# Kernel optimization log

Hardware: AMD Instinct MI355X
Metric: run time of the kernel (lower is better)

## Reference

```python
import jax, jax.numpy as jnp
import numpy as np

N = 100_000      # nodes
E = 1_600_000    # edges (avg degree 16)
F_IN = 128       # input features
H = 64           # hidden
C = 40           # classes


def setup_inputs() -> dict:
    key = jax.random.key(0)
    ks = jax.random.split(key, 12)
    s = 0.05
    return {
        "x": jax.random.normal(ks[0], (N, F_IN), dtype=jnp.float32),
        "edge_index": jax.random.randint(ks[1], (2, E), 0, N, dtype=jnp.int64),
        "edge_weight": jax.random.uniform(ks[2], (E,), dtype=jnp.float32),
        # first_lin: Linear(F_IN, H)
        "W_first": jax.random.normal(ks[3], (F_IN, H), dtype=jnp.float32) * s,
        "b_first": jnp.zeros((H,), jnp.float32),
        # convs[0], convs[1]: GCNConv(H, H)
        "W_c1": jax.random.normal(ks[4], (H, H), dtype=jnp.float32) * s,
        "b_c1": jnp.zeros((H,), jnp.float32),
        "W_c2": jax.random.normal(ks[5], (H, H), dtype=jnp.float32) * s,
        "b_c2": jnp.zeros((H,), jnp.float32),
        # lin2: Linear(H, C)
        "W_out": jax.random.normal(ks[6], (H, C), dtype=jnp.float32) * s,
        "b_out": jnp.zeros((C,), jnp.float32),
    }


def gcn_conv(h, edge_weight, row, col, W, b, n):
    """PyG GCNConv: h' = D^-1/2 (A + I) D^-1/2 (h W) + b, with edge weights."""
    h = h @ W                                        # [n, H]
    # add self-loops with weight 1
    loops = jnp.arange(n, dtype=row.dtype)
    row_sl = jnp.concatenate([row, loops])           # source nodes
    col_sl = jnp.concatenate([col, loops])           # target nodes
    ew_sl = jnp.concatenate([edge_weight, jnp.ones((n,), edge_weight.dtype)])
    # symmetric normalization
    deg = jax.ops.segment_sum(ew_sl, col_sl, num_segments=n)
    dinv = jnp.where(deg > 0, jax.lax.rsqrt(jnp.where(deg > 0, deg, 1.0)), 0.0)
    norm = dinv[row_sl] * ew_sl * dinv[col_sl]       # [E+n]
    # gather -> scale -> scatter-add at targets
    msgs = norm[:, None] * h[row_sl]                 # [E+n, H]
    out = jax.ops.segment_sum(msgs, col_sl, num_segments=n)
    return out + b


def reference(x, edge_index, edge_weight, W_first, b_first, W_c1, b_c1,
              W_c2, b_c2, W_out, b_out):
    row, col = edge_index[0], edge_index[1]
    n = x.shape[0]
    h = jax.nn.relu(x @ W_first + b_first)           # first_lin + relu (dropout eval no-op)
    h = jax.nn.relu(gcn_conv(h, edge_weight, row, col, W_c1, b_c1, n))
    h = jax.nn.relu(gcn_conv(h, edge_weight, row, col, W_c2, b_c2, n))
    logits = h @ W_out + b_out                       # lin2
    return jax.nn.log_softmax(logits, axis=-1)
```

## Files before the change

kernel.cpp:

```cpp
#include <hip/hip_runtime.h>
#include <hip/hip_bf16.h>
#include <cstdint>
#include <cstddef>

#define NN 100000
#define NE 1600000
#define FIN 128
#define HD 64
#define NC 40
#define NTILE (NN / 16)
#define MM_BLOCKS ((NTILE + 3) / 4)

#define BUK 256
#define NBUK ((NN + BUK - 1) / BUK)
#define EPB 1024
#define NBLK ((NE + EPB - 1) / EPB)

#define XSTR 68

typedef unsigned short u16;
typedef unsigned int u32;
typedef __attribute__((ext_vector_type(8))) short short8v;
typedef __attribute__((ext_vector_type(4))) float accf4;

__device__ __forceinline__ float u2lo(u32 u) { return __uint_as_float(u << 16); }
__device__ __forceinline__ float u2hi(u32 u) { return __uint_as_float(u & 0xFFFF0000u); }
__device__ __forceinline__ u16 f2b(float f) {
    u32 u = __float_as_uint(f);
    return (u16)((u + 0x7FFFu + ((u >> 16) & 1u)) >> 16);
}
__device__ __forceinline__ u32 pk2(float lo, float hi) {
    return (u32)f2b(lo) | ((u32)f2b(hi) << 16);
}

__launch_bounds__(256)
__global__ void k_build1(const int* __restrict__ ei, u32* __restrict__ hist,
                         const float* __restrict__ x, const float* __restrict__ W,
                         const float* __restrict__ b, u16* __restrict__ out) {
    if (blockIdx.x < NBLK) {
        __shared__ u32 lh[NBUK];
        int blk = blockIdx.x, tid = threadIdx.x;
        for (int i = tid; i < NBUK; i += 256) lh[i] = 0;
        __syncthreads();
        #pragma unroll
        for (int it = 0; it < EPB / 256; it++) {
            int e = blk * EPB + it * 256 + tid;
            if (e < NE) {
                int col = ei[NE + e];
                atomicAdd(&lh[col >> 8], 1u);
            }
        }
        __syncthreads();
        for (int i = tid; i < NBUK; i += 256) hist[(size_t)i * NBLK + blk] = lh[i];
        return;
    }
    __shared__ u32 xs[64 * XSTR];
    int tid = threadIdx.x;
    int bi  = blockIdx.x - NBLK;
    int nodeB = bi * 64;
    const float4* x4 = (const float4*)x;
    for (int idx = tid; idx < 64 * 16; idx += 256) {
        int row = idx >> 4, seg = idx & 15;
        uint4 d = make_uint4(0u, 0u, 0u, 0u);
        if (nodeB + row < NN) {
            float4 a = x4[(size_t)(nodeB + row) * 32 + seg * 2];
            float4 c = x4[(size_t)(nodeB + row) * 32 + seg * 2 + 1];
            d.x = pk2(a.x, a.y);
            d.y = pk2(a.z, a.w);
            d.z = pk2(c.x, c.y);
            d.w = pk2(c.z, c.w);
        }
        *(uint4*)(xs + row * XSTR + seg * 4) = d;
    }
    __syncthreads();
    int lane = tid & 63;
    int wv   = tid >> 6;
    int tile = bi * 4 + wv;
    if (tile >= NTILE) return;
    int row = lane & 15;
    int kg  = lane >> 4;
    short8v bW[4][4];
    #pragma unroll
    for (int kt = 0; kt < 4; kt++)
        #pragma unroll
        for (int ct = 0; ct < 4; ct++)
            #pragma unroll
            for (int j = 0; j < 8; j++)
                bW[kt][ct][j] = (short)f2b(W[(kt*32 + kg*8 + j) * HD + ct*16 + row]);
    int node0 = tile * 16;
    short8v af[4];
    #pragma unroll
    for (int kt = 0; kt < 4; kt++)
        af[kt] = *(const short8v*)(xs + (wv*16 + row) * XSTR + kt * 16 + kg * 4);
    accf4 acc[4] = {};
    #pragma unroll
    for (int kt = 0; kt < 4; kt++)
        #pragma unroll
        for (int ct = 0; ct < 4; ct++)
            acc[ct] = __builtin_amdgcn_mfma_f32_16x16x32_bf16(af[kt], bW[kt][ct], acc[ct], 0, 0, 0);
    #pragma unroll
    for (int ct = 0; ct < 4; ct++) {
        float bias = b[ct*16 + row];
        #pragma unroll
        for (int r = 0; r < 4; r++) {
            float v = fmaxf(acc[ct][r] + bias, 0.f);
            out[(size_t)(node0 + kg*4 + r) * HD + ct*16 + row] = f2b(v);
        }
    }
}

__global__ void k_bscan(u32* __restrict__ hist, u32* __restrict__ bucketTotal) {
    int b = blockIdx.x;
    int lane = threadIdx.x;
    u32* h = hist + (size_t)b * NBLK;
    u32 carry = 0;
    for (int j0 = 0; j0 < NBLK; j0 += 64) {
        int j = j0 + lane;
        u32 v = (j < NBLK) ? h[j] : 0;
        u32 inc = v;
        #pragma unroll
        for (int d = 1; d < 64; d <<= 1) {
            u32 t = __shfl_up(inc, d);
            if (lane >= d) inc += t;
        }
        if (j < NBLK) h[j] = carry + inc - v;
        carry += __shfl(inc, 63);
    }
    if (lane == 0) bucketTotal[b] = carry;
}

__global__ void k_bstart(const u32* __restrict__ bucketTotal, u32* __restrict__ bucketStart,
                         int* __restrict__ off) {
    int lane = threadIdx.x;
    u32 carry = 0;
    for (int j0 = 0; j0 < NBUK; j0 += 64) {
        int j = j0 + lane;
        u32 v = (j < NBUK) ? bucketTotal[j] : 0;
        u32 inc = v;
        #pragma unroll
        for (int d = 1; d < 64; d <<= 1) {
            u32 t = __shfl_up(inc, d);
            if (lane >= d) inc += t;
        }
        if (j < NBUK) bucketStart[j] = carry + inc - v;
        carry += __shfl(inc, 63);
    }
    if (lane == 0) { bucketStart[NBUK] = carry; off[NN] = (int)carry; }
}

__launch_bounds__(256)
__global__ void k_scatter(const int* __restrict__ ei, const float* __restrict__ ew,
                          const u32* __restrict__ hist, const u32* __restrict__ bucketStart,
                          uint2* __restrict__ rec) {
    __shared__ u32 lh[NBUK];
    __shared__ u32 gb[NBUK];
    int blk = blockIdx.x, tid = threadIdx.x;
    for (int i = tid; i < NBUK; i += 256) {
        lh[i] = 0;
        gb[i] = bucketStart[i] + hist[(size_t)i * NBLK + blk];
    }
    __syncthreads();
    #pragma unroll
    for (int it = 0; it < EPB / 256; it++) {
        int e = blk * EPB + it * 256 + tid;
        if (e < NE) {
            int row = ei[e], col = ei[NE + e];
            float wv = ew[e];
            int bkt = col >> 8;
            u32 cl = (u32)(col & 255);
            u32 r = atomicAdd(&lh[bkt], 1u);
            u32 slot = gb[bkt] + r;
            rec[slot] = make_uint2((u32)row | (cl << 24), __float_as_uint(wv));
        }
    }
}

__launch_bounds__(256)
__global__ void k_bucket(const uint2* __restrict__ rec, const u32* __restrict__ bucketStart,
                         float* __restrict__ dinv, int* __restrict__ off,
                         uint2* __restrict__ csr) {
    __shared__ u32 lpk[BUK];
    __shared__ u32 loff[BUK];
    __shared__ u32 wt[4];
    int b = blockIdx.x, tid = threadIdx.x;
    int base = b * BUK;
    u32 seg0 = bucketStart[b], seg1 = bucketStart[b + 1];
    int nb = (int)(seg1 - seg0);
    lpk[tid] = 0;
    __syncthreads();
    for (int idx = tid; idx < nb; idx += 256) {
        uint2 ab = rec[seg0 + idx];
        u32 cl = ab.x >> 24;
        u32 fx = __float2uint_rn(__uint_as_float(ab.y) * 16384.0f);
        atomicAdd(&lpk[cl], (1u << 20) | fx);
    }
    __syncthreads();
    u32 pk = lpk[tid];
    u32 cnt = pk >> 20;
    int node = base + tid;
    if (node < NN) dinv[node] = rsqrtf(1.0f + (float)(pk & 0xFFFFFu) * (1.0f / 16384.0f));
    int lane = tid & 63, wid = tid >> 6;
    u32 inc = cnt;
    #pragma unroll
    for (int d = 1; d < 64; d <<= 1) {
        u32 t = __shfl_up(inc, d);
        if (lane >= d) inc += t;
    }
    if (lane == 63) wt[wid] = inc;
    __syncthreads();
    u32 wof = 0;
    #pragma unroll
    for (int k = 0; k < 4; k++) if (k < wid) wof += wt[k];
    loff[tid] = wof + inc - cnt;
    if (node < NN) off[node] = (int)(seg0 + loff[tid]);
    lpk[tid] = 0;
    __syncthreads();
    for (int idx = tid; idx < nb; idx += 256) {
        uint2 ab = rec[seg0 + idx];
        u32 cl = ab.x >> 24;
        u32 r2 = atomicAdd(&lpk[cl], 1u);
        csr[seg0 + loff[cl] + r2] = make_uint2(ab.x & 0xFFFFFFu, ab.y);
    }
}

__launch_bounds__(256)
__global__ void k_mm64(const u16* __restrict__ A, const float* __restrict__ W,
                       const float* __restrict__ dinv, u16* __restrict__ out) {
    int lane = threadIdx.x & 63;
    int tile = blockIdx.x * 4 + (threadIdx.x >> 6);
    if (tile >= NTILE) return;
    int row = lane & 15;
    int kg  = lane >> 4;
    short8v bW[2][4];
    #pragma unroll
    for (int kt = 0; kt < 2; kt++)
        #pragma unroll
        for (int ct = 0; ct < 4; ct++)
            #pragma unroll
            for (int j = 0; j < 8; j++)
                bW[kt][ct][j] = (short)f2b(W[(kt*32 + kg*8 + j) * HD + ct*16 + row]);
    int node0 = tile * 16;
    const u16* ar = A + (size_t)(node0 + row) * HD + kg * 8;
    short8v af0 = *(const short8v*)(ar);
    short8v af1 = *(const short8v*)(ar + 32);
    accf4 acc[4] = {};
    #pragma unroll
    for (int ct = 0; ct < 4; ct++) {
        acc[ct] = __builtin_amdgcn_mfma_f32_16x16x32_bf16(af0, bW[0][ct], acc[ct], 0, 0, 0);
        acc[ct] = __builtin_amdgcn_mfma_f32_16x16x32_bf16(af1, bW[1][ct], acc[ct], 0, 0, 0);
    }
    float dr[4];
    #pragma unroll
    for (int r = 0; r < 4; r++) dr[r] = dinv[node0 + kg*4 + r];
    #pragma unroll
    for (int ct = 0; ct < 4; ct++)
        #pragma unroll
        for (int r = 0; r < 4; r++)
            out[(size_t)(node0 + kg*4 + r) * HD + ct*16 + row] = f2b(acc[ct][r] * dr[r]);
}

__launch_bounds__(256)
__global__ void k_agg(const uint4* __restrict__ Bm4, const int* __restrict__ off,
                      const uint2* __restrict__ csr, const float* __restrict__ dinv,
                      const float* __restrict__ bias, uint4* __restrict__ outp) {
    int lane = threadIdx.x & 63;
    int wave = threadIdx.x >> 6;
    int g    = lane >> 3;
    int fp   = lane & 7;
    int node = blockIdx.x * 32 + wave * 8 + g;
    int s = off[node], e = off[node + 1];
    int deg = e - s;
    float di = dinv[node];
    uint4 sw = Bm4[(size_t)node * 8 + fp];
    float a0 = u2lo(sw.x), a1 = u2hi(sw.x), a2 = u2lo(sw.y), a3 = u2hi(sw.y);
    float a4 = u2lo(sw.z), a5 = u2hi(sw.z), a6 = u2lo(sw.w), a7 = u2hi(sw.w);
    uint2 c0 = csr[s+0], c1 = csr[s+1], c2 = csr[s+2], c3 = csr[s+3];
    for (int j = 0; __any(j < deg); j += 4) {
        uint2 n0 = csr[s+j+4], n1 = csr[s+j+5], n2 = csr[s+j+6], n3 = csr[s+j+7];
        bool b0 = (j+0) < deg; u32 r0 = b0 ? c0.x : (u32)node; float w0 = b0 ? __uint_as_float(c0.y) : 0.f;
        bool b1 = (j+1) < deg; u32 r1 = b1 ? c1.x : (u32)node; float w1 = b1 ? __uint_as_float(c1.y) : 0.f;
        bool b2 = (j+2) < deg; u32 r2 = b2 ? c2.x : (u32)node; float w2 = b2 ? __uint_as_float(c2.y) : 0.f;
        bool b3 = (j+3) < deg; u32 r3 = b3 ? c3.x : (u32)node; float w3 = b3 ? __uint_as_float(c3.y) : 0.f;
        uint4 g0 = Bm4[(size_t)r0 * 8 + fp];
        uint4 g1 = Bm4[(size_t)r1 * 8 + fp];
        uint4 g2 = Bm4[(size_t)r2 * 8 + fp];
        uint4 g3 = Bm4[(size_t)r3 * 8 + fp];
        a0 += w0 * u2lo(g0.x) + w1 * u2lo(g1.x);
        a1 += w0 * u2hi(g0.x) + w1 * u2hi(g1.x);
        a2 += w0 * u2lo(g0.y) + w1 * u2lo(g1.y);
        a3 += w0 * u2hi(g0.y) + w1 * u2hi(g1.y);
        a4 += w0 * u2lo(g0.z) + w1 * u2lo(g1.z);
        a5 += w0 * u2hi(g0.z) + w1 * u2hi(g1.z);
        a6 += w0 * u2lo(g0.w) + w1 * u2lo(g1.w);
        a7 += w0 * u2hi(g0.w) + w1 * u2hi(g1.w);
        a0 += w2 * u2lo(g2.x) + w3 * u2lo(g3.x);
        a1 += w2 * u2hi(g2.x) + w3 * u2hi(g3.x);
        a2 += w2 * u2lo(g2.y) + w3 * u2lo(g3.y);
        a3 += w2 * u2hi(g2.y) + w3 * u2hi(g3.y);
        a4 += w2 * u2lo(g2.z) + w3 * u2lo(g3.z);
        a5 += w2 * u2hi(g2.z) + w3 * u2hi(g3.z);
        a6 += w2 * u2lo(g2.w) + w3 * u2lo(g3.w);
        a7 += w2 * u2hi(g2.w) + w3 * u2hi(g3.w);
        c0 = n0; c1 = n1; c2 = n2; c3 = n3;
    }
    float4 blo = *(const float4*)(bias + fp * 8);
    float4 bhi = *(const float4*)(bias + fp * 8 + 4);
    uint4 ov;
    ov.x = pk2(fmaxf(di * a0 + blo.x, 0.f), fmaxf(di * a1 + blo.y, 0.f));
    ov.y = pk2(fmaxf(di * a2 + blo.z, 0.f), fmaxf(di * a3 + blo.w, 0.f));
    ov.z = pk2(fmaxf(di * a4 + bhi.x, 0.f), fmaxf(di * a5 + bhi.y, 0.f));
    ov.w = pk2(fmaxf(di * a6 + bhi.z, 0.f), fmaxf(di * a7 + bhi.w, 0.f));
    outp[(size_t)node * 8 + fp] = ov;
}

__launch_bounds__(256)
__global__ void k_out(const u16* __restrict__ Hm, const float* __restrict__ W,
                      const float* __restrict__ b, float* __restrict__ outp) {
    int lane = threadIdx.x & 63;
    int tile = blockIdx.x * 4 + (threadIdx.x >> 6);
    if (tile >= NTILE) return;
    int row = lane & 15;
    int kg  = lane >> 4;
    short8v bW[2][3];
    #pragma unroll
    for (int kt = 0; kt < 2; kt++)
        #pragma unroll
        for (int ct = 0; ct < 3; ct++) {
            int col = ct*16 + row;
            #pragma unroll
            for (int j = 0; j < 8; j++)
                bW[kt][ct][j] = (col < NC) ? (short)f2b(W[(kt*32 + kg*8 + j) * NC + col]) : (short)0;
        }
    int node0 = tile * 16;
    const u16* ar = Hm + (size_t)(node0 + row) * HD + kg * 8;
    short8v af0 = *(const short8v*)(ar);
    short8v af1 = *(const short8v*)(ar + 32);
    accf4 acc[3] = {};
    #pragma unroll
    for (int ct = 0; ct < 3; ct++) {
        acc[ct] = __builtin_amdgcn_mfma_f32_16x16x32_bf16(af0, bW[0][ct], acc[ct], 0, 0, 0);
        acc[ct] = __builtin_amdgcn_mfma_f32_16x16x32_bf16(af1, bW[1][ct], acc[ct], 0, 0, 0);
    }
    float bias0 = b[row];
    float bias1 = b[16 + row];
    bool  has2  = (32 + row) < NC;
    float bias2 = has2 ? b[32 + row] : 0.f;
    #pragma unroll
    for (int r = 0; r < 4; r++) {
        float l0 = acc[0][r] + bias0;
        float l1 = acc[1][r] + bias1;
        float l2 = has2 ? acc[2][r] + bias2 : -1e30f;
        float m = fmaxf(fmaxf(l0, l1), l2);
        #pragma unroll
        for (int s2 = 8; s2 > 0; s2 >>= 1) m = fmaxf(m, __shfl_xor(m, s2));
        float sum = expf(l0 - m) + expf(l1 - m) + (has2 ? expf(l2 - m) : 0.f);
        #pragma unroll
        for (int s2 = 8; s2 > 0; s2 >>= 1) sum += __shfl_xor(sum, s2);
        float ls = logf(sum);
        size_t base = (size_t)(node0 + kg*4 + r) * NC;
        outp[base + row]      = (l0 - m) - ls;
        outp[base + 16 + row] = (l1 - m) - ls;
        if (has2) outp[base + 32 + row] = (l2 - m) - ls;
    }
}


extern "C" void kernel_launch(void* const* d_in, const int* in_sizes, int n_in,
                              void* d_out, int out_size, void* d_ws, size_t ws_size,
                              hipStream_t stream) {
    const float* x   = (const float*)d_in[0];
    const int*   ei  = (const int*)  d_in[1];
    const float* ew  = (const float*)d_in[2];
    const float* Wf  = (const float*)d_in[3];
    const float* bf  = (const float*)d_in[4];
    const float* Wc1 = (const float*)d_in[5];
    const float* bc1 = (const float*)d_in[6];
    const float* Wc2 = (const float*)d_in[7];
    const float* bc2 = (const float*)d_in[8];
    const float* Wo  = (const float*)d_in[9];
    const float* bo  = (const float*)d_in[10];
    float* out = (float*)d_out;

    char* w = (char*)d_ws;
    auto alloc = [&](size_t bytes) {
        char* p = w;
        w += (bytes + 511) & ~(size_t)511;
        return p;
    };
    u32*   hist = (u32*)  alloc((size_t)NBUK * NBLK * 4);
    u32*   btot = (u32*)  alloc((size_t)NBUK * 4);
    u32*   bst  = (u32*)  alloc((size_t)(NBUK + 1) * 4);
    float* dinv = (float*)alloc((size_t)NN * 4);
    int*   off  = (int*)  alloc((size_t)(NN + 1) * 4);
    uint2* rec  = (uint2*)alloc((size_t)NE * 8);
    uint2* csr  = (uint2*)alloc((size_t)(NE + 128) * 8);
    u16*   hA   = (u16*)  alloc((size_t)NN * HD * 2);
    u16*   hB   = (u16*)  alloc((size_t)NN * HD * 2);

    k_build1 <<<NBLK + MM_BLOCKS, 256, 0, stream>>>(ei, hist, x, Wf, bf, hA);
    k_bscan  <<<NBUK, 64, 0, stream>>>(hist, btot);
    k_bstart <<<1, 64, 0, stream>>>(btot, bst, off);
    k_scatter<<<NBLK, 256, 0, stream>>>(ei, ew, hist, bst, rec);
    k_bucket <<<NBUK, 256, 0, stream>>>(rec, bst, dinv, off, csr);

    k_mm64 <<<MM_BLOCKS, 256, 0, stream>>>(hA, Wc1, dinv, hB);
    k_agg  <<<NN / 32, 256, 0, stream>>>((const uint4*)hB, off, csr, dinv, bc1, (uint4*)hA);
    k_mm64 <<<MM_BLOCKS, 256, 0, stream>>>(hA, Wc2, dinv, hB);
    k_agg  <<<NN / 32, 256, 0, stream>>>((const uint4*)hB, off, csr, dinv, bc2, (uint4*)hA);
    k_out  <<<MM_BLOCKS, 256, 0, stream>>>(hA, Wo, bo, out);
}
```

Measured before the change: 186.5 us.

## Fuse aggregation with following matmul and output layer; transpose histogram layout

Fuses the first aggregation kernel with the second layer's 64x64 matmul, and fuses the second aggregation with the output linear plus log-softmax. Each block stages its 32 aggregated bf16 rows in shared memory and runs MFMA on them. This removes two kernel launches and the global round-trip of the hidden activations. The bucket histogram is also stored block-major, so histogram writes and the scatter reads are coalesced, while the scan kernel now reads with a stride. The cost is a block-wide barrier inside the gather kernels and per-block reloading of the weights.

Result: faster. 168.7 us (-9.5%).

```diff
diff --git a/kernel.cpp b/kernel.cpp
--- a/kernel.cpp
+++ b/kernel.cpp
@@ -17,6 +17,7 @@
 #define NBLK ((NE + EPB - 1) / EPB)
 
 #define XSTR 68
+#define HSTR 36
 
 typedef unsigned short u16;
 typedef unsigned int u32;
@@ -51,7 +52,8 @@
             }
         }
         __syncthreads();
-        for (int i = tid; i < NBUK; i += 256) hist[(size_t)i * NBLK + blk] = lh[i];
+        for (int i = tid; i < NBUK; i += 256)
+            hist[(size_t)blk * NBUK + i] = lh[i];
         return;
     }
     __shared__ u32 xs[64 * XSTR];
@@ -112,18 +114,17 @@
 __global__ void k_bscan(u32* __restrict__ hist, u32* __restrict__ bucketTotal) {
     int b = blockIdx.x;
     int lane = threadIdx.x;
-    u32* h = hist + (size_t)b * NBLK;
     u32 carry = 0;
     for (int j0 = 0; j0 < NBLK; j0 += 64) {
         int j = j0 + lane;
-        u32 v = (j < NBLK) ? h[j] : 0;
+        u32 v = (j < NBLK) ? hist[(size_t)j * NBUK + b] : 0;
         u32 inc = v;
         #pragma unroll
         for (int d = 1; d < 64; d <<= 1) {
             u32 t = __shfl_up(inc, d);
             if (lane >= d) inc += t;
         }
-        if (j < NBLK) h[j] = carry + inc - v;
+        if (j < NBLK) hist[(size_t)j * NBUK + b] = carry + inc - v;
         carry += __shfl(inc, 63);
     }
     if (lane == 0) bucketTotal[b] = carry;
@@ -157,7 +158,7 @@
     int blk = blockIdx.x, tid = threadIdx.x;
     for (int i = tid; i < NBUK; i += 256) {
         lh[i] = 0;
-        gb[i] = bucketStart[i] + hist[(size_t)i * NBLK + blk];
+        gb[i] = bucketStart[i] + hist[(size_t)blk * NBUK + i];
     }
     __syncthreads();
     #pragma unroll
@@ -260,9 +261,11 @@
 }
 
 __launch_bounds__(256)
-__global__ void k_agg(const uint4* __restrict__ Bm4, const int* __restrict__ off,
-                      const uint2* __restrict__ csr, const float* __restrict__ dinv,
-                      const float* __restrict__ bias, uint4* __restrict__ outp) {
+__global__ void k_aggmm(const uint4* __restrict__ Bm4, const int* __restrict__ off,
+                        const uint2* __restrict__ csr, const float* __restrict__ dinv,
+                        const float* __restrict__ bias, const float* __restrict__ W2,
+                        u16* __restrict__ tbl2) {
+    __shared__ u32 hs[32 * HSTR];
     int lane = threadIdx.x & 63;
     int wave = threadIdx.x >> 6;
     int g    = lane >> 3;
@@ -285,42 +288,109 @@
         uint4 g1 = Bm4[(size_t)r1 * 8 + fp];
         uint4 g2 = Bm4[(size_t)r2 * 8 + fp];
         uint4 g3 = Bm4[(size_t)r3 * 8 + fp];
-        a0 += w0 * u2lo(g0.x) + w1 * u2lo(g1.x);
-        a1 += w0 * u2hi(g0.x) + w1 * u2hi(g1.x);
-        a2 += w0 * u2lo(g0.y) + w1 * u2lo(g1.y);
-        a3 += w0 * u2hi(g0.y) + w1 * u2hi(g1.y);
-        a4 += w0 * u2lo(g0.z) + w1 * u2lo(g1.z);
-        a5 += w0 * u2hi(g0.z) + w1 * u2hi(g1.z);
-        a6 += w0 * u2lo(g0.w) + w1 * u2lo(g1.w);
-        a7 += w0 * u2hi(g0.w) + w1 * u2hi(g1.w);
-        a0 += w2 * u2lo(g2.x) + w3 * u2lo(g3.x);
-        a1 += w2 * u2hi(g2.x) + w3 * u2hi(g3.x);
-        a2 += w2 * u2lo(g2.y) + w3 * u2lo(g3.y);
-        a3 += w2 * u2hi(g2.y) + w3 * u2hi(g3.y);
-        a4 += w2 * u2lo(g2.z) + w3 * u2lo(g3.z);
-        a5 += w2 * u2hi(g2.z) + w3 * u2hi(g3.z);
-        a6 += w2 * u2lo(g2.w) + w3 * u2lo(g3.w);
-        a7 += w2 * u2hi(g2.w) + w3 * u2hi(g3.w);
+        a0 += w0*u2lo(g0.x) + w1*u2lo(g1.x) + w2*u2lo(g2.x) + w3*u2lo(g3.x);
+        a1 += w0*u2hi(g0.x) + w1*u2hi(g1.x) + w2*u2hi(g2.x) + w3*u2hi(g3.x);
+        a2 += w0*u2lo(g0.y) + w1*u2lo(g1.y) + w2*u2lo(g2.y) + w3*u2lo(g3.y);
+        a3 += w0*u2hi(g0.y) + w1*u2hi(g1.y) + w2*u2hi(g2.y) + w3*u2hi(g3.y);
+        a4 += w0*u2lo(g0.z) + w1*u2lo(g1.z) + w2*u2lo(g2.z) + w3*u2lo(g3.z);
+        a5 += w0*u2hi(g0.z) + w1*u2hi(g1.z) + w2*u2hi(g2.z) + w3*u2hi(g3.z);
+        a6 += w0*u2lo(g0.w) + w1*u2lo(g1.w) + w2*u2lo(g2.w) + w3*u2lo(g3.w);
+        a7 += w0*u2hi(g0.w) + w1*u2hi(g1.w) + w2*u2hi(g2.w) + w3*u2hi(g3.w);
         c0 = n0; c1 = n1; c2 = n2; c3 = n3;
     }
     float4 blo = *(const float4*)(bias + fp * 8);
     float4 bhi = *(const float4*)(bias + fp * 8 + 4);
-    uint4 ov;
-    ov.x = pk2(fmaxf(di * a0 + blo.x, 0.f), fmaxf(di * a1 + blo.y, 0.f));
-    ov.y = pk2(fmaxf(di * a2 + blo.z, 0.f), fmaxf(di * a3 + blo.w, 0.f));
-    ov.z = pk2(fmaxf(di * a4 + bhi.x, 0.f), fmaxf(di * a5 + bhi.y, 0.f));
-    ov.w = pk2(fmaxf(di * a6 + bhi.z, 0.f), fmaxf(di * a7 + bhi.w, 0.f));
-    outp[(size_t)node * 8 + fp] = ov;
-}
-
-__launch_bounds__(256)
-__global__ void k_out(const u16* __restrict__ Hm, const float* __restrict__ W,
-                      const float* __restrict__ b, float* __restrict__ outp) {
-    int lane = threadIdx.x & 63;
-    int tile = blockIdx.x * 4 + (threadIdx.x >> 6);
-    if (tile >= NTILE) return;
+    int lrow = wave * 8 + g;
+    uint4 hv;
+    hv.x = pk2(fmaxf(di*a0 + blo.x, 0.f), fmaxf(di*a1 + blo.y, 0.f));
+    hv.y = pk2(fmaxf(di*a2 + blo.z, 0.f), fmaxf(di*a3 + blo.w, 0.f));
+    hv.z = pk2(fmaxf(di*a4 + bhi.x, 0.f), fmaxf(di*a5 + bhi.y, 0.f));
+    hv.w = pk2(fmaxf(di*a6 + bhi.z, 0.f), fmaxf(di*a7 + bhi.w, 0.f));
+    *(uint4*)(hs + lrow * HSTR + fp * 4) = hv;
+    __syncthreads();
     int row = lane & 15;
     int kg  = lane >> 4;
+    int t      = wave & 1;
+    int ctbase = (wave >> 1) * 2;
+    short8v bW[2][2];
+    #pragma unroll
+    for (int kt = 0; kt < 2; kt++)
+        #pragma unroll
+        for (int cc = 0; cc < 2; cc++)
+            #pragma unroll
+            for (int j = 0; j < 8; j++)
+                bW[kt][cc][j] = (short)f2b(W2[(kt*32 + kg*8 + j) * HD + (ctbase+cc)*16 + row]);
+    short8v af0 = *(const short8v*)(hs + (t*16 + row) * HSTR + kg * 4);
+    short8v af1 = *(const short8v*)(hs + (t*16 + row) * HSTR + 16 + kg * 4);
+    accf4 acc[2] = {};
+    #pragma unroll
+    for (int cc = 0; cc < 2; cc++) {
+        acc[cc] = __builtin_amdgcn_mfma_f32_16x16x32_bf16(af0, bW[0][cc], acc[cc], 0, 0, 0);
+        acc[cc] = __builtin_amdgcn_mfma_f32_16x16x32_bf16(af1, bW[1][cc], acc[cc], 0, 0, 0);
+    }
+    int node0 = blockIdx.x * 32 + t * 16;
+    float dr[4];
+    #pragma unroll
+    for (int r = 0; r < 4; r++) dr[r] = dinv[node0 + kg*4 + r];
+    #pragma unroll
+    for (int cc = 0; cc < 2; cc++)
+        #pragma unroll
+        for (int r = 0; r < 4; r++)
+            tbl2[(size_t)(node0 + kg*4 + r) * HD + (ctbase+cc)*16 + row] = f2b(acc[cc][r] * dr[r]);
+}
+
+__launch_bounds__(256)
+__global__ void k_aggout(const uint4* __restrict__ Bm4, const int* __restrict__ off,
+                         const uint2* __restrict__ csr, const float* __restrict__ dinv,
+                         const float* __restrict__ bias, const float* __restrict__ Wo,
+                         const float* __restrict__ bo, float* __restrict__ outp) {
+    __shared__ u32 hs[32 * HSTR];
+    int lane = threadIdx.x & 63;
+    int wave = threadIdx.x >> 6;
+    int g    = lane >> 3;
+    int fp   = lane & 7;
+    int node = blockIdx.x * 32 + wave * 8 + g;
+    int s = off[node], e = off[node + 1];
+    int deg = e - s;
+    float di = dinv[node];
+    uint4 sw = Bm4[(size_t)node * 8 + fp];
+    float a0 = u2lo(sw.x), a1 = u2hi(sw.x), a2 = u2lo(sw.y), a3 = u2hi(sw.y);
+    float a4 = u2lo(sw.z), a5 = u2hi(sw.z), a6 = u2lo(sw.w), a7 = u2hi(sw.w);
+    uint2 c0 = csr[s+0], c1 = csr[s+1], c2 = csr[s+2], c3 = csr[s+3];
+    for (int j = 0; __any(j < deg); j += 4) {
+        uint2 n0 = csr[s+j+4], n1 = csr[s+j+5], n2 = csr[s+j+6], n3 = csr[s+j+7];
+        bool b0 = (j+0) < deg; u32 r0 = b0 ? c0.x : (u32)node; float w0 = b0 ? __uint_as_float(c0.y) : 0.f;
+        bool b1 = (j+1) < deg; u32 r1 = b1 ? c1.x : (u32)node; float w1 = b1 ? __uint_as_float(c1.y) : 0.f;
+        bool b2 = (j+2) < deg; u32 r2 = b2 ? c2.x : (u32)node; float w2 = b2 ? __uint_as_float(c2.y) : 0.f;
+        bool b3 = (j+3) < deg; u32 r3 = b3 ? c3.x : (u32)node; float w3 = b3 ? __uint_as_float(c3.y) : 0.f;
+        uint4 g0 = Bm4[(size_t)r0 * 8 + fp];
+        uint4 g1 = Bm4[(size_t)r1 * 8 + fp];
+        uint4 g2 = Bm4[(size_t)r2 * 8 + fp];
+        uint4 g3 = Bm4[(size_t)r3 * 8 + fp];
+        a0 += w0*u2lo(g0.x) + w1*u2lo(g1.x) + w2*u2lo(g2.x) + w3*u2lo(g3.x);
+        a1 += w0*u2hi(g0.x) + w1*u2hi(g1.x) + w2*u2hi(g2.x) + w3*u2hi(g3.x);
+        a2 += w0*u2lo(g0.y) + w1*u2lo(g1.y) + w2*u2lo(g2.y) + w3*u2lo(g3.y);
+        a3 += w0*u2hi(g0.y) + w1*u2hi(g1.y) + w2*u2hi(g2.y) + w3*u2hi(g3.y);
+        a4 += w0*u2lo(g0.z) + w1*u2lo(g1.z) + w2*u2lo(g2.z) + w3*u2lo(g3.z);
+        a5 += w0*u2hi(g0.z) + w1*u2hi(g1.z) + w2*u2hi(g2.z) + w3*u2hi(g3.z);
+        a6 += w0*u2lo(g0.w) + w1*u2lo(g1.w) + w2*u2lo(g2.w) + w3*u2lo(g3.w);
+        a7 += w0*u2hi(g0.w) + w1*u2hi(g1.w) + w2*u2hi(g2.w) + w3*u2hi(g3.w);
+        c0 = n0; c1 = n1; c2 = n2; c3 = n3;
+    }
+    float4 blo = *(const float4*)(bias + fp * 8);
+    float4 bhi = *(const float4*)(bias + fp * 8 + 4);
+    int lrow = wave * 8 + g;
+    uint4 hv;
+    hv.x = pk2(fmaxf(di*a0 + blo.x, 0.f), fmaxf(di*a1 + blo.y, 0.f));
+    hv.y = pk2(fmaxf(di*a2 + blo.z, 0.f), fmaxf(di*a3 + blo.w, 0.f));
+    hv.z = pk2(fmaxf(di*a4 + bhi.x, 0.f), fmaxf(di*a5 + bhi.y, 0.f));
+    hv.w = pk2(fmaxf(di*a6 + bhi.z, 0.f), fmaxf(di*a7 + bhi.w, 0.f));
+    *(uint4*)(hs + lrow * HSTR + fp * 4) = hv;
+    __syncthreads();
+    if (wave >= 2) return;
+    int row = lane & 15;
+    int kg  = lane >> 4;
+    int t = wave;
     short8v bW[2][3];
     #pragma unroll
     for (int kt = 0; kt < 2; kt++)
@@ -329,22 +399,21 @@
             int col = ct*16 + row;
             #pragma unroll
             for (int j = 0; j < 8; j++)
-                bW[kt][ct][j] = (col < NC) ? (short)f2b(W[(kt*32 + kg*8 + j) * NC + col]) : (short)0;
-        }
-    int node0 = tile * 16;
-    const u16* ar = Hm + (size_t)(node0 + row) * HD + kg * 8;
-    short8v af0 = *(const short8v*)(ar);
-    short8v af1 = *(const short8v*)(ar + 32);
+                bW[kt][ct][j] = (col < NC) ? (short)f2b(Wo[(kt*32 + kg*8 + j) * NC + col]) : (short)0;
+        }
+    short8v af0 = *(const short8v*)(hs + (t*16 + row) * HSTR + kg * 4);
+    short8v af1 = *(const short8v*)(hs + (t*16 + row) * HSTR + 16 + kg * 4);
     accf4 acc[3] = {};
     #pragma unroll
     for (int ct = 0; ct < 3; ct++) {
         acc[ct] = __builtin_amdgcn_mfma_f32_16x16x32_bf16(af0, bW[0][ct], acc[ct], 0, 0, 0);
         acc[ct] = __builtin_amdgcn_mfma_f32_16x16x32_bf16(af1, bW[1][ct], acc[ct], 0, 0, 0);
     }
-    float bias0 = b[row];
-    float bias1 = b[16 + row];
+    int node0 = blockIdx.x * 32 + t * 16;
+    float bias0 = bo[row];
+    float bias1 = bo[16 + row];
     bool  has2  = (32 + row) < NC;
-    float bias2 = has2 ? b[32 + row] : 0.f;
+    float bias2 = has2 ? bo[32 + row] : 0.f;
     #pragma unroll
     for (int r = 0; r < 4; r++) {
         float l0 = acc[0][r] + bias0;
@@ -387,7 +456,7 @@
         w += (bytes + 511) & ~(size_t)511;
         return p;
     };
-    u32*   hist = (u32*)  alloc((size_t)NBUK * NBLK * 4);
+    u32*   hist = (u32*)  alloc((size_t)NBLK * NBUK * 4);
     u32*   btot = (u32*)  alloc((size_t)NBUK * 4);
     u32*   bst  = (u32*)  alloc((size_t)(NBUK + 1) * 4);
     float* dinv = (float*)alloc((size_t)NN * 4);
@@ -403,9 +472,7 @@
     k_scatter<<<NBLK, 256, 0, stream>>>(ei, ew, hist, bst, rec);
     k_bucket <<<NBUK, 256, 0, stream>>>(rec, bst, dinv, off, csr);
 
-    k_mm64 <<<MM_BLOCKS, 256, 0, stream>>>(hA, Wc1, dinv, hB);
-    k_agg  <<<NN / 32, 256, 0, stream>>>((const uint4*)hB, off, csr, dinv, bc1, (uint4*)hA);
-    k_mm64 <<<MM_BLOCKS, 256, 0, stream>>>(hA, Wc2, dinv, hB);
-    k_agg  <<<NN / 32, 256, 0, stream>>>((const uint4*)hB, off, csr, dinv, bc2, (uint4*)hA);
-    k_out  <<<MM_BLOCKS, 256, 0, stream>>>(hA, Wo, bo, out);
-}
+    k_mm64  <<<MM_BLOCKS, 256, 0, stream>>>(hA, Wc1, dinv, hB);
+    k_aggmm <<<NN / 32, 256, 0, stream>>>((const uint4*)hB, off, csr, dinv, bc1, Wc2, hA);
+    k_aggout<<<NN / 32, 256, 0, stream>>>((const uint4*)hA, off, csr, dinv, bc2, Wo, bo, out);
+}
```
